# Performance work log

Measured on AMD Instinct MI355X. Metric: run time of the kernel, lower is better.

Reference implementation:

```python
import jax, jax.numpy as jnp
import numpy as np

K = 3
PAD = 1


def conv3x3(x, w):
    # x: [B,C,H,W], w: [O,C,3,3] -> [B,O,H,W], stride 1, pad 1, no bias
    return jax.lax.conv_general_dilated(
        x, w, window_strides=(1, 1), padding=((PAD, PAD), (PAD, PAD)),
        dimension_numbers=("NCHW", "OIHW", "NCHW"))


def bilinear_gather(x, py, px):
    """Zero-padded bilinear sampling (torchvision deform_conv2d semantics).
    x: [B,C,H,W]; py, px: [B,KK,H,W] absolute sampling coords.
    Returns [B,C,KK,H,W]."""
    B, C, H, W = x.shape
    KK = py.shape[1]
    y0 = jnp.floor(py)
    x0 = jnp.floor(px)
    wy1 = py - y0  # frac weights
    wx1 = px - x0
    wy0 = 1.0 - wy1
    wx0 = 1.0 - wx1
    x_flat = x.reshape(B, C, H * W)

    def corner(yi, xi, w):
        valid = (yi >= 0) & (yi <= H - 1) & (xi >= 0) & (xi <= W - 1)
        yc = jnp.clip(yi, 0, H - 1).astype(jnp.int32)
        xc = jnp.clip(xi, 0, W - 1).astype(jnp.int32)
        idx = (yc * W + xc).reshape(B, 1, KK * H * W)
        v = jnp.take_along_axis(x_flat, jnp.broadcast_to(idx, (B, C, KK * H * W)), axis=2)
        v = v.reshape(B, C, KK, H, W)
        return v * (w * valid.astype(x.dtype))[:, None]

    return (corner(y0, x0, wy0 * wx0) + corner(y0, x0 + 1.0, wy0 * wx1)
            + corner(y0 + 1.0, x0, wy1 * wx0) + corner(y0 + 1.0, x0 + 1.0, wy1 * wx1))


def deform_conv2d(x, offset, weight):
    """x: [B,C,H,W]; offset: [B,2*K*K,H,W] (dy,dx interleaved per tap, row-major);
    weight: [O,C,K,K]. stride 1, pad 1, dilation 1, 1 group, 1 offset group."""
    B, C, H, W = x.shape
    O = weight.shape[0]
    off = offset.reshape(B, K * K, 2, H, W)
    dy, dx = off[:, :, 0], off[:, :, 1]  # [B,9,H,W]
    ki, kj = jnp.meshgrid(jnp.arange(K, dtype=x.dtype), jnp.arange(K, dtype=x.dtype), indexing="ij")
    ki = ki.reshape(1, K * K, 1, 1)
    kj = kj.reshape(1, K * K, 1, 1)
    hh = jnp.arange(H, dtype=x.dtype).reshape(1, 1, H, 1)
    ww = jnp.arange(W, dtype=x.dtype).reshape(1, 1, 1, W)
    py = hh - PAD + ki + dy  # [B,9,H,W]
    px = ww - PAD + kj + dx
    sampled = bilinear_gather(x, py, px)  # [B,C,9,H,W]
    return jnp.einsum("bckhw,ock->bohw", sampled, weight.reshape(O, C, K * K))


def offset_estimator(x, w1, w2, w3):
    # channel-preserving bottleneck stand-in for Dynamic_offset_estimator
    h = jax.nn.relu(conv3x3(x, w1))
    h = jax.nn.relu(conv3x3(h, w2))
    return conv3x3(h, w3)


def setup_inputs() -> dict:
    key = jax.random.key(0)
    ks = jax.random.split(key, 7)
    B, C, H, W = 1, 768, 64, 64
    C2, CM = 2 * C, 192
    f32 = jnp.float32
    inp = {
        "input_features": jax.random.normal(ks[0], (B, C, H, W), dtype=f32),
        "reference_features": jax.random.normal(ks[1], (B, C, H, W), dtype=f32),
        "est_w1": jax.random.normal(ks[2], (CM, C2, K, K), dtype=f32) / np.sqrt(C2 * K * K),
        "est_w2": jax.random.normal(ks[3], (CM, CM, K, K), dtype=f32) / np.sqrt(CM * K * K),
        "est_w3": jax.random.normal(ks[4], (C2, CM, K, K), dtype=f32) / np.sqrt(CM * K * K),
        "offset_w": jax.random.normal(ks[5], (18, C2, K, K), dtype=f32) / np.sqrt(C2 * K * K),
        "deform_w": jax.random.normal(ks[6], (C, C, K, K), dtype=f32) / np.sqrt(C * K * K),
    }
    return inp


def reference(input_features, reference_features, est_w1, est_w2, est_w3, offset_w, deform_w):
    input_offset = jnp.concatenate([input_features, reference_features], axis=1)  # [B,2C,H,W]
    est = offset_estimator(input_offset, est_w1, est_w2, est_w3)  # [B,2C,H,W]
    offset = conv3x3(est, offset_w)  # [B,18,H,W]
    return deform_conv2d(reference_features, offset, deform_w)  # [B,C,H,W]
```

## Files before the change

kernel.cpp:

```cpp
#include <hip/hip_runtime.h>

#define HWPX 4096

typedef short s8v  __attribute__((ext_vector_type(8)));
typedef float f4v  __attribute__((ext_vector_type(4)));

__device__ inline unsigned short f2bf(float f) {
    unsigned u = __float_as_uint(f);
    return (unsigned short)((u + 0x7fffu + ((u >> 16) & 1u)) >> 16);
}
__device__ inline float bf2f(unsigned s) {
    return __uint_as_float(s << 16);
}

#define GLDS16(gsrc, ldst) \
    __builtin_amdgcn_global_load_lds( \
        (const __attribute__((address_space(1))) unsigned int*)(gsrc), \
        (__attribute__((address_space(3))) unsigned int*)(ldst), 16, 0, 0)

#define C1 2654208
#define C2 2985984
#define C3 5640192
#define C4 6082560
#define C5 11390976

__device__ __forceinline__ void wpack_wave(const float* __restrict__ src,
                                           short* __restrict__ dst,
                                           int g, int cb, int f, int lane,
                                           int Cin, int Cout, int S, int NB)
{
    const int lm = lane & 15, quad = lane >> 4;
    const int cout = g * (NB * 16) + f * 16 + lm;
    float r[72];
    if (cout < Cout) {
        const float* p = src + ((size_t)cout * Cin + cb * 32) * 9 + quad * 72;
#pragma unroll
        for (int j = 0; j < 18; ++j) {
            float4 v = *(const float4*)(p + j * 4);
            r[j * 4 + 0] = v.x; r[j * 4 + 1] = v.y;
            r[j * 4 + 2] = v.z; r[j * 4 + 3] = v.w;
        }
    } else {
#pragma unroll
        for (int j = 0; j < 72; ++j) r[j] = 0.f;
    }
#pragma unroll
    for (int t = 0; t < 9; ++t) {
        uint4 o;
        o.x = f2bf(r[0 * 9 + t]) | ((unsigned)f2bf(r[1 * 9 + t]) << 16);
        o.y = f2bf(r[2 * 9 + t]) | ((unsigned)f2bf(r[3 * 9 + t]) << 16);
        o.z = f2bf(r[4 * 9 + t]) | ((unsigned)f2bf(r[5 * 9 + t]) << 16);
        o.w = f2bf(r[6 * 9 + t]) | ((unsigned)f2bf(r[7 * 9 + t]) << 16);
        *(uint4*)&dst[((size_t)(g * S + cb * 9 + t) * NB + f) * 512 + lane * 8] = o;
    }
}

__global__ __launch_bounds__(256)
void prep_k(const float* __restrict__ xa, const float* __restrict__ xb,
            short* __restrict__ xt,
            const float* __restrict__ s1, const float* __restrict__ s2,
            const float* __restrict__ s3, const float* __restrict__ s4,
            const float* __restrict__ s5,
            short* __restrict__ d1, short* __restrict__ d2,
            short* __restrict__ d3, short* __restrict__ d4,
            short* __restrict__ d5)
{
    __shared__ __align__(16) short T[64 * 72];
    const int tid = threadIdx.x;
    if (blockIdx.x < 1536) {
        const int b = blockIdx.x;
        const int c0 = (b % 24) * 64, p0 = (b / 24) * 64;
        for (int i = tid; i < 4096; i += 256) {
            int cl = i >> 6, pl = i & 63;
            int c = c0 + cl;
            float v = (c < 768) ? xa[(size_t)c * HWPX + p0 + pl]
                                : xb[(size_t)(c - 768) * HWPX + p0 + pl];
            T[pl * 72 + cl] = (short)f2bf(v);
        }
        __syncthreads();
        for (int i = tid; i < 512; i += 256) {
            int pl = i >> 3, part = i & 7;
            uint4 v = *(const uint4*)&T[pl * 72 + part * 8];
            *(uint4*)&xt[(size_t)(p0 + pl) * 1536 + c0 + part * 8] = v;
        }
    } else {
        const int wid = (blockIdx.x - 1536) * 4 + (tid >> 6);
        const int lane = tid & 63;
        if (wid < 576) {
            int id = wid;
            wpack_wave(s1, d1, id / 192, (id / 4) % 48, id & 3, lane, 1536, 192, 432, 4);
        } else if (wid < 648) {
            int id = wid - 576;
            wpack_wave(s2, d2, id / 12, (id / 2) % 6, id & 1, lane, 192, 192, 54, 2);
        } else if (wid < 1224) {
            int id = wid - 648;
            wpack_wave(s3, d3, id / 24, (id / 4) % 6, id & 3, lane, 192, 1536, 54, 4);
        } else if (wid < 1320) {
            int id = wid - 1224;
            wpack_wave(s4, d4, id / 96, (id / 2) % 48, id & 1, lane, 1536, 18, 432, 2);
        } else if (wid < 2472) {
            int id = wid - 1320;
            wpack_wave(s5, d5, id / 96, (id / 4) % 24, id & 3, lane, 768, 768, 216, 4);
        }
    }
}

template<int NB, bool SUM2>
__global__ __launch_bounds__(256, 3)
void convf_k(const short* __restrict__ Xt, const short* __restrict__ Xt2,
             int CinStr,
             const short* __restrict__ Wp, int S, int chunks,
             short* __restrict__ Out, int Cstr, int splitStride)
{
    __shared__ __align__(16) short sH[6 * 66 * 40];
    const int tid = threadIdx.x, lane = tid & 63, wv = tid >> 6;
    const int lm = lane & 15, quad = lane >> 4;
    const int r0 = blockIdx.x * 4;
    const int g  = blockIdx.y;
    const int cb0 = blockIdx.z * chunks;
    short* out = Out + (size_t)blockIdx.z * splitStride;

    f4v acc[4][NB];
#pragma unroll
    for (int ma = 0; ma < 4; ++ma)
#pragma unroll
        for (int nb = 0; nb < NB; ++nb)
#pragma unroll
            for (int r = 0; r < 4; ++r) acc[ma][nb][r] = 0.f;

    for (int cc = 0; cc < chunks; ++cc) {
        const int cb = cb0 + cc;
        const short* wpB = Wp + ((size_t)(g * S + cb * 9) * NB) * 512 + lane * 8;
        s8v bb[NB];
#pragma unroll
        for (int f = 0; f < NB; ++f)
            bb[f] = *(const s8v*)&wpB[(size_t)f * 512];

        for (int i = tid; i < 1584; i += 256) {
            int slot = i >> 2, part = i & 3;
            int hr = slot / 66, px = slot % 66;
            int gy = r0 - 1 + hr, gx = px - 1;
            uint4 v = {0, 0, 0, 0};
            if (gy >= 0 && gy < 64 && gx >= 0 && gx < 64) {
                size_t base = (size_t)(gy * 64 + gx) * CinStr + cb * 32 + part * 8;
                v = *(const uint4*)&Xt[base];
                if (SUM2) {
                    uint4 v2 = *(const uint4*)&Xt2[base];
                    unsigned* a = (unsigned*)&v;
                    const unsigned* b = (const unsigned*)&v2;
#pragma unroll
                    for (int k = 0; k < 4; ++k) {
                        float lo = bf2f(a[k] & 0xffffu) + bf2f(b[k] & 0xffffu);
                        float hi = bf2f(a[k] >> 16)     + bf2f(b[k] >> 16);
                        a[k] = f2bf(lo) | ((unsigned)f2bf(hi) << 16);
                    }
                }
            }
            *(uint4*)&sH[slot * 40 + part * 8] = v;
        }
        __syncthreads();

#pragma unroll
        for (int t = 0; t < 9; ++t) {
            const int ty = t / 3, tx = t % 3;
            s8v nxt[NB];
#pragma unroll
            for (int f = 0; f < NB; ++f)
                nxt[f] = *(const s8v*)&wpB[(size_t)((t + 1) * NB + f) * 512];
            s8v a[4];
#pragma unroll
            for (int ma = 0; ma < 4; ++ma)
                a[ma] = *(const s8v*)&sH[((wv + ty) * 66 + ma * 16 + lm + tx) * 40 + quad * 8];
#pragma unroll
            for (int ma = 0; ma < 4; ++ma)
#pragma unroll
                for (int nb = 0; nb < NB; ++nb)
                    acc[ma][nb] = __builtin_amdgcn_mfma_f32_16x16x32_bf16(
                        a[ma], bb[nb], acc[ma][nb], 0, 0, 0);
#pragma unroll
            for (int f = 0; f < NB; ++f) bb[f] = nxt[f];
        }
        __syncthreads();
    }

    const int py = (r0 + wv) * 64;
#pragma unroll
    for (int ma = 0; ma < 4; ++ma)
#pragma unroll
        for (int nb = 0; nb < NB; ++nb)
#pragma unroll
            for (int r = 0; r < 4; ++r)
                out[(size_t)(py + ma * 16 + quad * 4 + r) * Cstr
                    + g * (NB * 16) + nb * 16 + lm] = (short)f2bf(acc[ma][nb][r]);
}

__global__ __launch_bounds__(256)
void ep_sumb_k(const short* __restrict__ P, short* __restrict__ outb,
               int nsplit, size_t splitStride, int n8, int relu)
{
    int i = blockIdx.x * 256 + threadIdx.x;
    if (i >= n8) return;
    size_t base = (size_t)i * 8;
    float s[8];
#pragma unroll
    for (int j = 0; j < 8; ++j) s[j] = 0.f;
    for (int sp = 0; sp < nsplit; ++sp) {
        uint4 v = *(const uint4*)&P[sp * splitStride + base];
        s[0] += bf2f(v.x & 0xffffu); s[1] += bf2f(v.x >> 16);
        s[2] += bf2f(v.y & 0xffffu); s[3] += bf2f(v.y >> 16);
        s[4] += bf2f(v.z & 0xffffu); s[5] += bf2f(v.z >> 16);
        s[6] += bf2f(v.w & 0xffffu); s[7] += bf2f(v.w >> 16);
    }
    if (relu) {
#pragma unroll
        for (int j = 0; j < 8; ++j) s[j] = fmaxf(s[j], 0.f);
    }
    uint4 o;
    o.x = f2bf(s[0]) | ((unsigned)f2bf(s[1]) << 16);
    o.y = f2bf(s[2]) | ((unsigned)f2bf(s[3]) << 16);
    o.z = f2bf(s[4]) | ((unsigned)f2bf(s[5]) << 16);
    o.w = f2bf(s[6]) | ((unsigned)f2bf(s[7]) << 16);
    *(uint4*)&outb[base] = o;
}

__global__ __launch_bounds__(256)
void ep_offs_k(const short* __restrict__ P, float* __restrict__ offs, int nsplit)
{
    int i = blockIdx.x * 256 + threadIdx.x;
    if (i >= 18 * HWPX) return;
    int m = i >> 12, px = i & 4095;
    float s = 0.f;
    for (int sp = 0; sp < nsplit; ++sp)
        s += bf2f((unsigned short)P[((size_t)sp * HWPX + px) * 32 + m]);
    offs[i] = s;
}

__global__ __launch_bounds__(256)
void sample_k(const short* __restrict__ xcat, const float* __restrict__ offs,
              short* __restrict__ Smp)
{
    __shared__ int   s_mi[9][16][4];
    __shared__ float s_mw[9][16][4];
    const int tid = threadIdx.x;
    const int p0  = blockIdx.x * 16;
    const int cbq = blockIdx.y * 6;
    const int wv  = tid >> 6, lane = tid & 63;
    const int lmx = lane & 15, qd = lane >> 4;
    const int pg  = p0 >> 6, ma = (p0 >> 4) & 3;

    if (tid < 144) {
        int t = tid / 16, p = tid % 16;
        int pxg = p0 + p;
        int r = pxg >> 6, x = pxg & 63;
        float dy = offs[(size_t)(2 * t)     * HWPX + pxg];
        float dx = offs[(size_t)(2 * t + 1) * HWPX + pxg];
        float py  = (float)(r - 1 + t / 3) + dy;
        float pxf = (float)(x - 1 + t % 3) + dx;
        py  = fminf(fmaxf(py,  -1e6f), 1e6f);
        pxf = fminf(fmaxf(pxf, -1e6f), 1e6f);
        float y0f = floorf(py), x0f = floorf(pxf);
        float wy1 = py - y0f, wx1 = pxf - x0f;
        float wy0 = 1.f - wy1, wx0 = 1.f - wx1;
        bool vy0 = (y0f >=  0.f) && (y0f <= 63.f);
        bool vy1 = (y0f >= -1.f) && (y0f <= 62.f);
        bool vx0 = (x0f >=  0.f) && (x0f <= 63.f);
        bool vx1 = (x0f >= -1.f) && (x0f <= 62.f);
        int y0 = (int)fminf(fmaxf(y0f,       0.f), 63.f);
        int y1 = (int)fminf(fmaxf(y0f + 1.f, 0.f), 63.f);
        int x0 = (int)fminf(fmaxf(x0f,       0.f), 63.f);
        int x1 = (int)fminf(fmaxf(x0f + 1.f, 0.f), 63.f);
        s_mi[t][p][0] = y0 * 64 + x0;  s_mw[t][p][0] = (vy0 && vx0) ? wy0 * wx0 : 0.f;
        s_mi[t][p][1] = y0 * 64 + x1;  s_mw[t][p][1] = (vy0 && vx1) ? wy0 * wx1 : 0.f;
        s_mi[t][p][2] = y1 * 64 + x0;  s_mw[t][p][2] = (vy1 && vx0) ? wy1 * wx0 : 0.f;
        s_mi[t][p][3] = y1 * 64 + x1;  s_mw[t][p][3] = (vy1 && vx1) ? wy1 * wx1 : 0.f;
    }
    __syncthreads();

    for (int j = wv; j < 54; j += 4) {
        const int t = j / 6, cb = cbq + j % 6;
        int   mi[4];
        float mw[4];
#pragma unroll
        for (int c = 0; c < 4; ++c) {
            mi[c] = s_mi[t][lmx][c];
            mw[c] = s_mw[t][lmx][c];
        }
        float a[8];
#pragma unroll
        for (int k = 0; k < 8; ++k) a[k] = 0.f;
#pragma unroll
        for (int c = 0; c < 4; ++c) {
            float wgt = mw[c];
            const short* src = xcat + (size_t)mi[c] * 1536 + 768 + cb * 32 + qd * 8;
            uint4 v = *(const uint4*)src;
            a[0] += wgt * bf2f(v.x & 0xffffu); a[1] += wgt * bf2f(v.x >> 16);
            a[2] += wgt * bf2f(v.y & 0xffffu); a[3] += wgt * bf2f(v.y >> 16);
            a[4] += wgt * bf2f(v.z & 0xffffu); a[5] += wgt * bf2f(v.z >> 16);
            a[6] += wgt * bf2f(v.w & 0xffffu); a[7] += wgt * bf2f(v.w >> 16);
        }
        uint4 o;
        o.x = f2bf(a[0]) | ((unsigned)f2bf(a[1]) << 16);
        o.y = f2bf(a[2]) | ((unsigned)f2bf(a[3]) << 16);
        o.z = f2bf(a[4]) | ((unsigned)f2bf(a[5]) << 16);
        o.w = f2bf(a[6]) | ((unsigned)f2bf(a[7]) << 16);
        size_t addr = ((((size_t)pg * 216 + cb * 9 + t) * 4 + ma) * 64 + lane) * 8;
        *(uint4*)&Smp[addr] = o;
    }
}

__global__ __launch_bounds__(256, 3)
void dgemm_k(const short* __restrict__ Ap, const short* __restrict__ Bp,
             short* __restrict__ P)
{
    __shared__ __align__(16) short sL[3 * 8192];

    const int tid = threadIdx.x, lane = tid & 63, wv = tid >> 6;
    const int lm = lane & 15, quad = lane >> 4;
    const int mg = blockIdx.y * 2 + (wv >> 1);
    const int pg = blockIdx.x * 2 + (wv & 1);
    const int s0 = blockIdx.z * 54;

    const short* stSrc;
    int stChunk;
    if (wv < 2) {
        stSrc = Ap + ((size_t)(blockIdx.y * 2 + wv) * 216 + s0) * 2048;
        stChunk = wv * 2048;
    } else {
        stSrc = Bp + ((size_t)(blockIdx.x * 2 + (wv - 2)) * 216 + s0) * 2048;
        stChunk = 4096 + (wv - 2) * 2048;
    }

    f4v acc[4][4];
#pragma unroll
    for (int ma = 0; ma < 4; ++ma)
#pragma unroll
        for (int nb = 0; nb < 4; ++nb)
#pragma unroll
            for (int r = 0; r < 4; ++r) acc[ma][nb][r] = 0.f;

#pragma unroll
    for (int j = 0; j < 4; ++j)
        GLDS16(stSrc + (size_t)0 * 2048 + j * 512 + lane * 8,
               &sL[0 * 8192 + stChunk + j * 512]);
#pragma unroll
    for (int j = 0; j < 4; ++j)
        GLDS16(stSrc + (size_t)1 * 2048 + j * 512 + lane * 8,
               &sL[1 * 8192 + stChunk + j * 512]);
    asm volatile("s_waitcnt vmcnt(4)" ::: "memory");
    __builtin_amdgcn_s_barrier();
    __builtin_amdgcn_sched_barrier(0);

    const int aOff = (wv >> 1) * 2048;
    const int bOff = 4096 + (wv & 1) * 2048;

    s8v avA[4], bvA[4], avB[4], bvB[4];
#pragma unroll
    for (int f = 0; f < 4; ++f) {
        avA[f] = *(const s8v*)&sL[0 * 8192 + aOff + f * 512 + lane * 8];
        bvA[f] = *(const s8v*)&sL[0 * 8192 + bOff + f * 512 + lane * 8];
    }

    int cA = 0, cB = 1, cC = 2;

    for (int s = 0; s < 52; s += 2) {
#pragma unroll
        for (int j = 0; j < 4; ++j)
            GLDS16(stSrc + (size_t)(s + 2) * 2048 + j * 512 + lane * 8,
                   &sL[cC * 8192 + stChunk + j * 512]);
        asm volatile("s_waitcnt vmcnt(4)" ::: "memory");
        __builtin_amdgcn_s_barrier();
        __builtin_amdgcn_sched_barrier(0);
        {
            const int base = cB * 8192;
#pragma unroll
            for (int f = 0; f < 4; ++f) {
                avB[f] = *(const s8v*)&sL[base + aOff + f * 512 + lane * 8];
                bvB[f] = *(const s8v*)&sL[base + bOff + f * 512 + lane * 8];
            }
        }
#pragma unroll
        for (int ma = 0; ma < 4; ++ma)
#pragma unroll
            for (int nb = 0; nb < 4; ++nb)
                acc[ma][nb] = __builtin_amdgcn_mfma_f32_16x16x32_bf16(
                    avA[ma], bvA[nb], acc[ma][nb], 0, 0, 0);

#pragma unroll
        for (int j = 0; j < 4; ++j)
            GLDS16(stSrc + (size_t)(s + 3) * 2048 + j * 512 + lane * 8,
                   &sL[cA * 8192 + stChunk + j * 512]);
        asm volatile("s_waitcnt vmcnt(4)" ::: "memory");
        __builtin_amdgcn_s_barrier();
        __builtin_amdgcn_sched_barrier(0);
        {
            const int base = cC * 8192;
#pragma unroll
            for (int f = 0; f < 4; ++f) {
                avA[f] = *(const s8v*)&sL[base + aOff + f * 512 + lane * 8];
                bvA[f] = *(const s8v*)&sL[base + bOff + f * 512 + lane * 8];
            }
        }
#pragma unroll
        for (int ma = 0; ma < 4; ++ma)
#pragma unroll
            for (int nb = 0; nb < 4; ++nb)
                acc[ma][nb] = __builtin_amdgcn_mfma_f32_16x16x32_bf16(
                    avB[ma], bvB[nb], acc[ma][nb], 0, 0, 0);

        int nA = cC, nB = cA, nC = cB;
        cA = nA; cB = nB; cC = nC;
    }

    asm volatile("s_waitcnt vmcnt(0)" ::: "memory");
    __builtin_amdgcn_s_barrier();
    __builtin_amdgcn_sched_barrier(0);
    {
        const int base = cB * 8192;
#pragma unroll
        for (int f = 0; f < 4; ++f) {
            avB[f] = *(const s8v*)&sL[base + aOff + f * 512 + lane * 8];
            bvB[f] = *(const s8v*)&sL[base + bOff + f * 512 + lane * 8];
        }
    }
#pragma unroll
    for (int ma = 0; ma < 4; ++ma)
#pragma unroll
        for (int nb = 0; nb < 4; ++nb)
            acc[ma][nb] = __builtin_amdgcn_mfma_f32_16x16x32_bf16(
                avA[ma], bvA[nb], acc[ma][nb], 0, 0, 0);
#pragma unroll
    for (int ma = 0; ma < 4; ++ma)
#pragma unroll
        for (int nb = 0; nb < 4; ++nb)
            acc[ma][nb] = __builtin_amdgcn_mfma_f32_16x16x32_bf16(
                avB[ma], bvB[nb], acc[ma][nb], 0, 0, 0);

    short* p = P + (size_t)blockIdx.z * 768 * HWPX;
#pragma unroll
    for (int ma = 0; ma < 4; ++ma)
#pragma unroll
        for (int nb = 0; nb < 4; ++nb)
#pragma unroll
            for (int r = 0; r < 4; ++r)
                p[(size_t)(mg * 64 + ma * 16 + quad * 4 + r) * HWPX
                  + pg * 64 + nb * 16 + lm] = (short)f2bf(acc[ma][nb][r]);
}

__global__ __launch_bounds__(256)
void ep_dg_k(const short* __restrict__ P, float* __restrict__ out)
{
    int i = blockIdx.x * 256 + threadIdx.x;
    if (i >= 768 * HWPX / 8) return;
    size_t base = (size_t)i * 8;
    float s[8];
#pragma unroll
    for (int j = 0; j < 8; ++j) s[j] = 0.f;
    for (int sp = 0; sp < 4; ++sp) {
        uint4 v = *(const uint4*)&P[(size_t)sp * 768 * HWPX + base];
        s[0] += bf2f(v.x & 0xffffu); s[1] += bf2f(v.x >> 16);
        s[2] += bf2f(v.y & 0xffffu); s[3] += bf2f(v.y >> 16);
        s[4] += bf2f(v.z & 0xffffu); s[5] += bf2f(v.z >> 16);
        s[6] += bf2f(v.w & 0xffffu); s[7] += bf2f(v.w >> 16);
    }
    float4 o0 = make_float4(s[0], s[1], s[2], s[3]);
    float4 o1 = make_float4(s[4], s[5], s[6], s[7]);
    *(float4*)&out[base]     = o0;
    *(float4*)&out[base + 4] = o1;
}

extern "C" void kernel_launch(void* const* d_in, const int* in_sizes, int n_in,
                              void* d_out, int out_size, void* d_ws, size_t ws_size,
                              hipStream_t stream)
{
    const float* x_in  = (const float*)d_in[0];
    const float* x_ref = (const float*)d_in[1];
    const float* w1    = (const float*)d_in[2];
    const float* w2    = (const float*)d_in[3];
    const float* w3    = (const float*)d_in[4];
    const float* ow    = (const float*)d_in[5];
    const float* dw    = (const float*)d_in[6];
    float* out = (float*)d_out;

    char* w = (char*)d_ws;
    size_t off = 0;
    auto carve = [&](size_t bytes) {
        void* p = w + off;
        off += (bytes + 255) & ~(size_t)255;
        return p;
    };
    short* xcat = (short*)carve((size_t)4096 * 1536 * 2);
    short* w1p  = (short*)carve((size_t)C1 * 2);
    short* w2p  = (short*)carve((size_t)(C2 - C1) * 2);
    short* w3p  = (short*)carve((size_t)(C3 - C2) * 2);
    short* w4p  = (short*)carve((size_t)(C4 - C3) * 2);
    short* dwp  = (short*)carve((size_t)(C5 - C4) * 2);
    float* offs = (float*)carve((size_t)18 * 4096 * 4);
    short* Smp  = (short*)carve((size_t)4096 * 6912 * 2);
    char*  R    = (char*)carve((size_t)2 * 768 * 4096 * 4);
    short* rh1  = (short*)R;
    short* rh2  = (short*)(R + 1572864);
    short* p4   = (short*)(R + 3145728);
    short* Pcv  = Smp;
    short* Pdg  = (short*)R;

    prep_k<<<1536 + 618, 256, 0, stream>>>(
        x_in, x_ref, xcat, w1, w2, w3, ow, dw, w1p, w2p, w3p, w4p, dwp);

    const int n8 = 4096 * 192 / 8;
    convf_k<4, false><<<dim3(16, 3, 16), 256, 0, stream>>>(
        xcat, nullptr, 1536, w1p, 432, 3, Pcv, 192, 4096 * 192);
    ep_sumb_k<<<(n8 + 255) / 256, 256, 0, stream>>>(Pcv, rh1, 16, (size_t)4096 * 192, n8, 1);
    convf_k<2, false><<<dim3(16, 6, 6), 256, 0, stream>>>(
        rh1, nullptr, 192, w2p, 54, 1, Pcv, 192, 4096 * 192);
    ep_sumb_k<<<(n8 + 255) / 256, 256, 0, stream>>>(Pcv, rh2, 6, (size_t)4096 * 192, n8, 1);
    convf_k<4, false><<<dim3(16, 24, 2), 256, 0, stream>>>(
        rh2, nullptr, 192, w3p, 54, 3, Pcv, 1536, 4096 * 1536);
    convf_k<2, true><<<dim3(16, 1, 48), 256, 0, stream>>>(
        Pcv, Pcv + (size_t)4096 * 1536, 1536, w4p, 432, 1, p4, 32, 4096 * 32);
    ep_offs_k<<<(18 * HWPX + 255) / 256, 256, 0, stream>>>(p4, offs, 48);
    sample_k<<<dim3(256, 4), 256, 0, stream>>>(xcat, offs, Smp);
    dgemm_k<<<dim3(32, 6, 4), 256, 0, stream>>>(dwp, Smp, Pdg);
    ep_dg_k<<<(768 * HWPX / 8 + 255) / 256, 256, 0, stream>>>(Pdg, out);
}
```

Measured before the change: 305.6 us.

## Load A fragments directly to registers and stage only B through LDS

In the deformable-conv GEMM kernel, each wave now loads its own A (weight) fragments straight from global memory into registers, prefetched one step ahead. Only the B (sampled-input) tiles, which are shared between the two row-group waves, still go through LDS, so the LDS buffers shrink by half and the staging loads are spread over all four waves. This removes LDS traffic and shared-memory footprint for A, which each wave uses alone. The cost is more outstanding global loads per wave, more registers, and reliance on vmcnt ordering for correctness.

New measurement: 315.9 us. 1.03x slower.

```diff
diff --git a/kernel.cpp b/kernel.cpp
--- a/kernel.cpp
+++ b/kernel.cpp
@@ -312,7 +312,7 @@
 void dgemm_k(const short* __restrict__ Ap, const short* __restrict__ Bp,
              short* __restrict__ P)
 {
-    __shared__ __align__(16) short sL[3 * 8192];
+    __shared__ __align__(16) short sL[3 * 4096];
 
     const int tid = threadIdx.x, lane = tid & 63, wv = tid >> 6;
     const int lm = lane & 15, quad = lane >> 4;
@@ -320,14 +320,17 @@
     const int pg = blockIdx.x * 2 + (wv & 1);
     const int s0 = blockIdx.z * 54;
 
-    const short* stSrc;
-    int stChunk;
-    if (wv < 2) {
-        stSrc = Ap + ((size_t)(blockIdx.y * 2 + wv) * 216 + s0) * 2048;
-        stChunk = wv * 2048;
-    } else {
-        stSrc = Bp + ((size_t)(blockIdx.x * 2 + (wv - 2)) * 216 + s0) * 2048;
-        stChunk = 4096 + (wv - 2) * 2048;
+    const short* ap = Ap + ((size_t)(mg * 216 + s0) * 4) * 512 + lane * 8;
+
+    const short* stSrc[2];
+    int stDst[2];
+#pragma unroll
+    for (int u = 0; u < 2; ++u) {
+        int o = wv * 2 + u;
+        int c = o >> 2, j = o & 3;
+        stSrc[u] = Bp + ((size_t)((blockIdx.x * 2 + c) * 216 + s0) * 4) * 512
+                 + j * 512 + lane * 8;
+        stDst[u] = c * 2048 + j * 512;
     }
 
     f4v acc[4][4];
@@ -339,101 +342,90 @@
             for (int r = 0; r < 4; ++r) acc[ma][nb][r] = 0.f;
 
 #pragma unroll
-    for (int j = 0; j < 4; ++j)
-        GLDS16(stSrc + (size_t)0 * 2048 + j * 512 + lane * 8,
-               &sL[0 * 8192 + stChunk + j * 512]);
-#pragma unroll
-    for (int j = 0; j < 4; ++j)
-        GLDS16(stSrc + (size_t)1 * 2048 + j * 512 + lane * 8,
-               &sL[1 * 8192 + stChunk + j * 512]);
-    asm volatile("s_waitcnt vmcnt(4)" ::: "memory");
-    __builtin_amdgcn_s_barrier();
-    __builtin_amdgcn_sched_barrier(0);
-
-    const int aOff = (wv >> 1) * 2048;
-    const int bOff = 4096 + (wv & 1) * 2048;
-
-    s8v avA[4], bvA[4], avB[4], bvB[4];
-#pragma unroll
-    for (int f = 0; f < 4; ++f) {
-        avA[f] = *(const s8v*)&sL[0 * 8192 + aOff + f * 512 + lane * 8];
-        bvA[f] = *(const s8v*)&sL[0 * 8192 + bOff + f * 512 + lane * 8];
-    }
-
-    int cA = 0, cB = 1, cC = 2;
-
-    for (int s = 0; s < 52; s += 2) {
-#pragma unroll
-        for (int j = 0; j < 4; ++j)
-            GLDS16(stSrc + (size_t)(s + 2) * 2048 + j * 512 + lane * 8,
-                   &sL[cC * 8192 + stChunk + j * 512]);
-        asm volatile("s_waitcnt vmcnt(4)" ::: "memory");
-        __builtin_amdgcn_s_barrier();
-        __builtin_amdgcn_sched_barrier(0);
-        {
-            const int base = cB * 8192;
-#pragma unroll
-            for (int f = 0; f < 4; ++f) {
-                avB[f] = *(const s8v*)&sL[base + aOff + f * 512 + lane * 8];
-                bvB[f] = *(const s8v*)&sL[base + bOff + f * 512 + lane * 8];
-            }
-        }
-#pragma unroll
-        for (int ma = 0; ma < 4; ++ma)
-#pragma unroll
-            for (int nb = 0; nb < 4; ++nb)
-                acc[ma][nb] = __builtin_amdgcn_mfma_f32_16x16x32_bf16(
-                    avA[ma], bvA[nb], acc[ma][nb], 0, 0, 0);
-
-#pragma unroll
-        for (int j = 0; j < 4; ++j)
-            GLDS16(stSrc + (size_t)(s + 3) * 2048 + j * 512 + lane * 8,
-                   &sL[cA * 8192 + stChunk + j * 512]);
-        asm volatile("s_waitcnt vmcnt(4)" ::: "memory");
-        __builtin_amdgcn_s_barrier();
-        __builtin_amdgcn_sched_barrier(0);
-        {
-            const int base = cC * 8192;
-#pragma unroll
-            for (int f = 0; f < 4; ++f) {
-                avA[f] = *(const s8v*)&sL[base + aOff + f * 512 + lane * 8];
-                bvA[f] = *(const s8v*)&sL[base + bOff + f * 512 + lane * 8];
-            }
-        }
-#pragma unroll
-        for (int ma = 0; ma < 4; ++ma)
-#pragma unroll
-            for (int nb = 0; nb < 4; ++nb)
-                acc[ma][nb] = __builtin_amdgcn_mfma_f32_16x16x32_bf16(
-                    avB[ma], bvB[nb], acc[ma][nb], 0, 0, 0);
-
-        int nA = cC, nB = cA, nC = cB;
-        cA = nA; cB = nB; cC = nC;
-    }
-
+    for (int u = 0; u < 2; ++u)
+        GLDS16(stSrc[u], &sL[0 * 4096 + stDst[u]]);
+#pragma unroll
+    for (int u = 0; u < 2; ++u)
+        GLDS16(stSrc[u] + 2048, &sL[1 * 4096 + stDst[u]]);
+    s8v a0[4], a1[4], u0[4], u1[4];
+#pragma unroll
+    for (int f = 0; f < 4; ++f)
+        a0[f] = *(const s8v*)&ap[f * 512];
     asm volatile("s_waitcnt vmcnt(0)" ::: "memory");
     __builtin_amdgcn_s_barrier();
     __builtin_amdgcn_sched_barrier(0);
-    {
-        const int base = cB * 8192;
-#pragma unroll
-        for (int f = 0; f < 4; ++f) {
-            avB[f] = *(const s8v*)&sL[base + aOff + f * 512 + lane * 8];
-            bvB[f] = *(const s8v*)&sL[base + bOff + f * 512 + lane * 8];
-        }
-    }
+
+    const int bOff = (wv & 1) * 2048;
+#pragma unroll
+    for (int f = 0; f < 4; ++f)
+        u0[f] = *(const s8v*)&sL[0 * 4096 + bOff + f * 512 + lane * 8];
+
+    int cA = 0, cB = 1, cC = 2;
+
+    for (int s = 0; s < 52; s += 2) {
+#pragma unroll
+        for (int f = 0; f < 4; ++f)
+            a1[f] = *(const s8v*)&ap[(size_t)(s + 1) * 2048 + f * 512];
+#pragma unroll
+        for (int u = 0; u < 2; ++u)
+            GLDS16(stSrc[u] + (size_t)(s + 2) * 2048, &sL[cC * 4096 + stDst[u]]);
+        asm volatile("s_waitcnt vmcnt(6)" ::: "memory");
+        __builtin_amdgcn_s_barrier();
+        __builtin_amdgcn_sched_barrier(0);
+#pragma unroll
+        for (int f = 0; f < 4; ++f)
+            u1[f] = *(const s8v*)&sL[cB * 4096 + bOff + f * 512 + lane * 8];
+#pragma unroll
+        for (int ma = 0; ma < 4; ++ma)
+#pragma unroll
+            for (int nb = 0; nb < 4; ++nb)
+                acc[ma][nb] = __builtin_amdgcn_mfma_f32_16x16x32_bf16(
+                    a0[ma], u0[nb], acc[ma][nb], 0, 0, 0);
+
+#pragma unroll
+        for (int f = 0; f < 4; ++f)
+            a0[f] = *(const s8v*)&ap[(size_t)(s + 2) * 2048 + f * 512];
+#pragma unroll
+        for (int u = 0; u < 2; ++u)
+            GLDS16(stSrc[u] + (size_t)(s + 3) * 2048, &sL[cA * 4096 + stDst[u]]);
+        asm volatile("s_waitcnt vmcnt(6)" ::: "memory");
+        __builtin_amdgcn_s_barrier();
+        __builtin_amdgcn_sched_barrier(0);
+#pragma unroll
+        for (int f = 0; f < 4; ++f)
+            u0[f] = *(const s8v*)&sL[cC * 4096 + bOff + f * 512 + lane * 8];
+#pragma unroll
+        for (int ma = 0; ma < 4; ++ma)
+#pragma unroll
+            for (int nb = 0; nb < 4; ++nb)
+                acc[ma][nb] = __builtin_amdgcn_mfma_f32_16x16x32_bf16(
+                    a1[ma], u1[nb], acc[ma][nb], 0, 0, 0);
+
+        int nA = cC, nB = cA, nC = cB;
+        cA = nA; cB = nB; cC = nC;
+    }
+
+#pragma unroll
+    for (int f = 0; f < 4; ++f)
+        a1[f] = *(const s8v*)&ap[(size_t)53 * 2048 + f * 512];
+    asm volatile("s_waitcnt vmcnt(0)" ::: "memory");
+    __builtin_amdgcn_s_barrier();
+    __builtin_amdgcn_sched_barrier(0);
+#pragma unroll
+    for (int f = 0; f < 4; ++f)
+        u1[f] = *(const s8v*)&sL[cB * 4096 + bOff + f * 512 + lane * 8];
 #pragma unroll
     for (int ma = 0; ma < 4; ++ma)
 #pragma unroll
         for (int nb = 0; nb < 4; ++nb)
             acc[ma][nb] = __builtin_amdgcn_mfma_f32_16x16x32_bf16(
-                avA[ma], bvA[nb], acc[ma][nb], 0, 0, 0);
+                a0[ma], u0[nb], acc[ma][nb], 0, 0, 0);
 #pragma unroll
     for (int ma = 0; ma < 4; ++ma)
 #pragma unroll
         for (int nb = 0; nb < 4; ++nb)
             acc[ma][nb] = __builtin_amdgcn_mfma_f32_16x16x32_bf16(
-                avB[ma], bvB[nb], acc[ma][nb], 0, 0, 0);
+                a1[ma], u1[nb], acc[ma][nb], 0, 0, 0);
 
     short* p = P + (size_t)blockIdx.z * 768 * HWPX;
 #pragma unroll
```
